# Kernel optimization log

Hardware: AMD Instinct MI355X
Metric: run time of the kernel (lower is better)

Reference implementation:

```python
import jax, jax.numpy as jnp
import numpy as np

B, S, D, H = 2, 48, 256, 8
DH = D // H  # depth per head = 32
N = S * S    # flattened pair sequence length = 2304


def setup_inputs() -> dict:
    key = jax.random.key(0)
    ks = jax.random.split(key, 9)
    std = 1.0 / np.sqrt(D)
    x = jax.random.normal(ks[0], (B, S, S, D), dtype=jnp.float32)
    Wq = jax.random.normal(ks[1], (D, D), dtype=jnp.float32) * std
    Wk = jax.random.normal(ks[2], (D, D), dtype=jnp.float32) * std
    Wv = jax.random.normal(ks[3], (D, D), dtype=jnp.float32) * std
    Wo = jax.random.normal(ks[4], (D, D), dtype=jnp.float32) * std
    bq = jnp.zeros((D,), jnp.float32)
    bk = jnp.zeros((D,), jnp.float32)
    bv = jnp.zeros((D,), jnp.float32)
    bo = jnp.zeros((D,), jnp.float32)
    return {"pair_representation": x, "Wq": Wq, "bq": bq, "Wk": Wk, "bk": bk,
            "Wv": Wv, "bv": bv, "Wo": Wo, "bo": bo}


def reference(pair_representation, Wq, bq, Wk, bk, Wv, bv, Wo, bo):
    x = pair_representation.reshape(B, N, D)  # flatten (S,S) -> N

    def heads(t):  # (B,N,D) -> (B,H,N,DH)
        return t.reshape(B, N, H, DH).transpose(0, 2, 1, 3)

    q = heads(x @ Wq + bq)
    k = heads(x @ Wk + bk)
    v = heads(x @ Wv + bv)

    scale = 1.0 / jnp.sqrt(jnp.asarray(DH, jnp.float32))
    logits = jnp.einsum('bhnd,bhmd->bhnm', q, k) * scale  # (B,H,N,N)
    attn = jax.nn.softmax(logits, axis=-1)
    ctx = jnp.einsum('bhnm,bhmd->bhnd', attn, v)
    ctx = ctx.transpose(0, 2, 1, 3).reshape(B, N, D)
    return ctx @ Wo + bo  # (B, N, D)
```

## Files before the change

kernel.cpp:

```cpp
#include <hip/hip_runtime.h>
#include <math.h>

#define B 2
#define S 48
#define D 256
#define H 8
#define DH 32
#define N (S*S)
#define BN (B*N)
#define BH (B*H)
#define KS 6
#define KPZ (N/KS)
#define NE ((size_t)BN*D)
#define BHN (BH*N)

typedef _Float16 half8 __attribute__((ext_vector_type(8)));
typedef _Float16 half4_t __attribute__((ext_vector_type(4)));
typedef unsigned short ushort8_t __attribute__((ext_vector_type(8)));
typedef float floatx4 __attribute__((ext_vector_type(4)));

__device__ __forceinline__ void split8(const float* v, half8* hi, half8* lo) {
    #pragma unroll
    for (int j = 0; j < 8; j++) {
        _Float16 h = (_Float16)v[j];
        (*hi)[j] = h;
        (*lo)[j] = (_Float16)(v[j] - (float)h);
    }
}

__global__ __launch_bounds__(256) void proj_kernel(
    const float* __restrict__ x,
    const float* __restrict__ Wq, const float* __restrict__ bq,
    const float* __restrict__ Wk, const float* __restrict__ bk,
    const float* __restrict__ Wv, const float* __restrict__ bv,
    _Float16* __restrict__ qbuf, _Float16* __restrict__ kbuf,
    _Float16* __restrict__ vtbuf)
{
    __shared__ __align__(16) _Float16 AhS[64 * 72];
    __shared__ __align__(16) _Float16 AlS[64 * 72];
    __shared__ __align__(16) _Float16 BhS[64 * 72];
    __shared__ __align__(16) _Float16 BlS[64 * 72];

    const int z = blockIdx.z;
    const float* W    = (z == 0) ? Wq : (z == 1) ? Wk : Wv;
    const float* bias = (z == 0) ? bq : (z == 1) ? bk : bv;
    const float scale = (z == 0) ? rsqrtf((float)DH) * 1.44269504f : 1.0f;

    const int t = threadIdx.x;
    const int wv2 = t >> 6, lane = t & 63, l15 = lane & 15, quad = lane >> 4;
    const int rowb = blockIdx.x * 64;
    const int colb = blockIdx.y * 64;
    floatx4 acc[4] = {{0,0,0,0},{0,0,0,0},{0,0,0,0},{0,0,0,0}};

    for (int kb0 = 0; kb0 < D; kb0 += 64) {
        __syncthreads();
        #pragma unroll
        for (int i = 0; i < 2; i++) {
            int idx = i * 2048 + t * 8;
            int r = idx >> 6, c = idx & 63;
            const float* xp = x + (size_t)(rowb + r) * D + kb0 + c;
            float4 x0 = *(const float4*)xp;
            float4 x1 = *(const float4*)(xp + 4);
            float v[8] = {x0.x, x0.y, x0.z, x0.w, x1.x, x1.y, x1.z, x1.w};
            half8 hi, lo;
            split8(v, &hi, &lo);
            *(half8*)(AhS + r * 72 + c) = hi;
            *(half8*)(AlS + r * 72 + c) = lo;
        }
        #pragma unroll
        for (int i = 0; i < 2; i++) {
            int u = i * 256 + t;
            int cc = u & 63, k0 = (u >> 6) * 8;
            float v[8];
            #pragma unroll
            for (int j = 0; j < 8; j++)
                v[j] = W[(size_t)(kb0 + k0 + j) * D + colb + cc];
            half8 hi, lo;
            split8(v, &hi, &lo);
            *(half8*)(BhS + cc * 72 + k0) = hi;
            *(half8*)(BlS + cc * 72 + k0) = lo;
        }
        __syncthreads();
        #pragma unroll
        for (int ksx = 0; ksx < 2; ksx++) {
            half8 ah = *(const half8*)(AhS + (wv2 * 16 + l15) * 72 + ksx * 32 + quad * 8);
            half8 al = *(const half8*)(AlS + (wv2 * 16 + l15) * 72 + ksx * 32 + quad * 8);
            #pragma unroll
            for (int cg = 0; cg < 4; cg++) {
                half8 bh8 = *(const half8*)(BhS + (cg * 16 + l15) * 72 + ksx * 32 + quad * 8);
                half8 bl8 = *(const half8*)(BlS + (cg * 16 + l15) * 72 + ksx * 32 + quad * 8);
                acc[cg] = __builtin_amdgcn_mfma_f32_16x16x32_f16(ah, bh8, acc[cg], 0, 0, 0);
                acc[cg] = __builtin_amdgcn_mfma_f32_16x16x32_f16(al, bh8, acc[cg], 0, 0, 0);
                acc[cg] = __builtin_amdgcn_mfma_f32_16x16x32_f16(ah, bl8, acc[cg], 0, 0, 0);
            }
        }
    }

    const int bb = (rowb >= N) ? 1 : 0;
    #pragma unroll
    for (int cg = 0; cg < 4; cg++) {
        int col = colb + cg * 16 + l15;
        int hh = col >> 5, dh = col & 31;
        float bs = bias[col];
        if (z < 2) {
            _Float16* op = (z == 0) ? qbuf : kbuf;
            #pragma unroll
            for (int r = 0; r < 4; r++) {
                int n = rowb + wv2 * 16 + quad * 4 + r - bb * N;
                float v = (acc[cg][r] + bs) * scale;
                op[((size_t)(bb * H + hh) * N + n) * DH + dh] = (_Float16)v;
            }
        } else {
            int n0 = rowb + wv2 * 16 + quad * 4 - bb * N;
            half4_t pk;
            #pragma unroll
            for (int r = 0; r < 4; r++) pk[r] = (_Float16)(acc[cg][r] + bs);
            *(half4_t*)(vtbuf + ((size_t)(bb * H + hh) * DH + dh) * N + n0) = pk;
        }
    }
}

__global__ __launch_bounds__(256) void attn_kernel(
    const _Float16* __restrict__ qbuf, const _Float16* __restrict__ kbuf,
    const _Float16* __restrict__ vtbuf,
    float* __restrict__ ctx_part, float* __restrict__ lpart)
{
    __shared__ __align__(16) _Float16 Ks[64 * 40];
    __shared__ __align__(16) _Float16 Vt[32 * 72];

    const int t = threadIdx.x;
    const int wv2 = t >> 6, lane = t & 63, l15 = lane & 15, quad = lane >> 4;
    const int bh = blockIdx.y, kz = blockIdx.z;
    const int qbase = blockIdx.x * 128 + wv2 * 32;

    half8 bq8[2];
    #pragma unroll
    for (int qg = 0; qg < 2; qg++)
        bq8[qg] = *(const half8*)(qbuf +
            ((size_t)bh * N + qbase + qg * 16 + l15) * DH + quad * 8);

    floatx4 acc[2][2] = {{{0,0,0,0},{0,0,0,0}},{{0,0,0,0},{0,0,0,0}}};
    float lsum[2] = {0.f, 0.f};

    const int skey = t >> 2, sd0 = (t & 3) * 8;
    const int svd = t >> 3, svk = (t & 7) * 8;

    for (int it = 0; it < KPZ / 64; it++) {
        const int key0 = kz * KPZ + it * 64;
        __syncthreads();
        *(ushort8_t*)(Ks + skey * 40 + sd0) =
            *(const ushort8_t*)(kbuf + ((size_t)bh * N + key0 + skey) * DH + sd0);
        *(ushort8_t*)(Vt + svd * 72 + svk) =
            *(const ushort8_t*)(vtbuf + ((size_t)bh * DH + svd) * N + key0 + svk);
        __syncthreads();

        #pragma unroll
        for (int kg = 0; kg < 4; kg++) {
            half8 ka = *(const half8*)(Ks + (kg * 16 + l15) * 40 + quad * 8);
            half4_t va0 = *(const half4_t*)(Vt + l15 * 72 + kg * 16 + quad * 4);
            half4_t va1 = *(const half4_t*)(Vt + (16 + l15) * 72 + kg * 16 + quad * 4);
            #pragma unroll
            for (int qg = 0; qg < 2; qg++) {
                floatx4 s = {0, 0, 0, 0};
                s = __builtin_amdgcn_mfma_f32_16x16x32_f16(ka, bq8[qg], s, 0, 0, 0);
                half4_t pf;
                #pragma unroll
                for (int r = 0; r < 4; r++) {
                    float p = exp2f(s[r]);
                    lsum[qg] += p;
                    pf[r] = (_Float16)p;
                }
                acc[qg][0] = __builtin_amdgcn_mfma_f32_16x16x16f16(va0, pf, acc[qg][0], 0, 0, 0);
                acc[qg][1] = __builtin_amdgcn_mfma_f32_16x16x16f16(va1, pf, acc[qg][1], 0, 0, 0);
            }
        }
    }

    const int bb = bh >> 3, hh = bh & 7;
    #pragma unroll
    for (int qg = 0; qg < 2; qg++) {
        float ls = lsum[qg];
        ls += __shfl_xor(ls, 16);
        ls += __shfl_xor(ls, 32);
        int q = qbase + qg * 16 + l15;
        if (quad == 0) lpart[(size_t)kz * BHN + bh * N + q] = ls;
        float* crow = ctx_part + (size_t)kz * NE + ((size_t)bb * N + q) * D + hh * DH;
        *(floatx4*)(crow + quad * 4)      = acc[qg][0];
        *(floatx4*)(crow + 16 + quad * 4) = acc[qg][1];
    }
}

__global__ __launch_bounds__(256) void outproj_kernel(
    const float* __restrict__ ctx_part, const float* __restrict__ lpart,
    const float* __restrict__ Wo, const float* __restrict__ bo,
    float* __restrict__ out)
{
    __shared__ __align__(16) _Float16 AhS[64 * 72];
    __shared__ __align__(16) _Float16 AlS[64 * 72];
    __shared__ __align__(16) _Float16 BhS[64 * 72];
    __shared__ __align__(16) _Float16 BlS[64 * 72];

    const int t = threadIdx.x;
    const int wv2 = t >> 6, lane = t & 63, l15 = lane & 15, quad = lane >> 4;
    const int rowb = blockIdx.x * 64;
    const int colb = blockIdx.y * 64;
    floatx4 acc[4] = {{0,0,0,0},{0,0,0,0},{0,0,0,0},{0,0,0,0}};

    for (int kb0 = 0; kb0 < D; kb0 += 64) {
        __syncthreads();
        #pragma unroll
        for (int i = 0; i < 2; i++) {
            int idx = i * 2048 + t * 8;
            int r = idx >> 6, c = idx & 63;
            int row = rowb + r;
            int kcol = kb0 + c;
            int bb = (row >= N) ? 1 : 0;
            int n = row - bb * N;
            int bhn = (bb * H + (kcol >> 5)) * N + n;
            float ls = 0.f;
            #pragma unroll
            for (int zz = 0; zz < KS; zz++) ls += lpart[(size_t)zz * BHN + bhn];
            float inv = 1.0f / ls;
            float v[8] = {};
            #pragma unroll
            for (int zz = 0; zz < KS; zz++) {
                const float* pp = ctx_part + (size_t)zz * NE + (size_t)row * D + kcol;
                float4 p0 = *(const float4*)pp;
                float4 p1 = *(const float4*)(pp + 4);
                v[0] += p0.x; v[1] += p0.y; v[2] += p0.z; v[3] += p0.w;
                v[4] += p1.x; v[5] += p1.y; v[6] += p1.z; v[7] += p1.w;
            }
            #pragma unroll
            for (int j = 0; j < 8; j++) v[j] *= inv;
            half8 hi, lo;
            split8(v, &hi, &lo);
            *(half8*)(AhS + r * 72 + c) = hi;
            *(half8*)(AlS + r * 72 + c) = lo;
        }
        #pragma unroll
        for (int i = 0; i < 2; i++) {
            int u = i * 256 + t;
            int cc = u & 63, k0 = (u >> 6) * 8;
            float v[8];
            #pragma unroll
            for (int j = 0; j < 8; j++)
                v[j] = Wo[(size_t)(kb0 + k0 + j) * D + colb + cc];
            half8 hi, lo;
            split8(v, &hi, &lo);
            *(half8*)(BhS + cc * 72 + k0) = hi;
            *(half8*)(BlS + cc * 72 + k0) = lo;
        }
        __syncthreads();
        #pragma unroll
        for (int ksx = 0; ksx < 2; ksx++) {
            half8 ah = *(const half8*)(AhS + (wv2 * 16 + l15) * 72 + ksx * 32 + quad * 8);
            half8 al = *(const half8*)(AlS + (wv2 * 16 + l15) * 72 + ksx * 32 + quad * 8);
            #pragma unroll
            for (int cg = 0; cg < 4; cg++) {
                half8 bh8 = *(const half8*)(BhS + (cg * 16 + l15) * 72 + ksx * 32 + quad * 8);
                half8 bl8 = *(const half8*)(BlS + (cg * 16 + l15) * 72 + ksx * 32 + quad * 8);
                acc[cg] = __builtin_amdgcn_mfma_f32_16x16x32_f16(ah, bh8, acc[cg], 0, 0, 0);
                acc[cg] = __builtin_amdgcn_mfma_f32_16x16x32_f16(al, bh8, acc[cg], 0, 0, 0);
                acc[cg] = __builtin_amdgcn_mfma_f32_16x16x32_f16(ah, bl8, acc[cg], 0, 0, 0);
            }
        }
    }

    #pragma unroll
    for (int cg = 0; cg < 4; cg++) {
        int col = colb + cg * 16 + l15;
        float bs = bo[col];
        #pragma unroll
        for (int r = 0; r < 4; r++) {
            int row = rowb + wv2 * 16 + quad * 4 + r;
            out[(size_t)row * D + col] = acc[cg][r] + bs;
        }
    }
}

extern "C" void kernel_launch(void* const* d_in, const int* in_sizes, int n_in,
                              void* d_out, int out_size, void* d_ws, size_t ws_size,
                              hipStream_t stream)
{
    const float* x  = (const float*)d_in[0];
    const float* Wq = (const float*)d_in[1];
    const float* bq = (const float*)d_in[2];
    const float* Wk = (const float*)d_in[3];
    const float* bk = (const float*)d_in[4];
    const float* Wv = (const float*)d_in[5];
    const float* bv = (const float*)d_in[6];
    const float* Wo = (const float*)d_in[7];
    const float* bo = (const float*)d_in[8];
    float* out = (float*)d_out;

    float* ctx_part = (float*)d_ws;
    float* lpart    = ctx_part + (size_t)KS * NE;
    _Float16* qbuf  = (_Float16*)(lpart + (size_t)KS * BHN);
    _Float16* kbuf  = qbuf + NE;
    _Float16* vtbuf = kbuf + NE;

    proj_kernel<<<dim3(BN / 64, D / 64, 3), 256, 0, stream>>>(
        x, Wq, bq, Wk, bk, Wv, bv, qbuf, kbuf, vtbuf);

    attn_kernel<<<dim3(N / 128, BH, KS), 256, 0, stream>>>(
        qbuf, kbuf, vtbuf, ctx_part, lpart);

    outproj_kernel<<<dim3(BN / 64, D / 64), 256, 0, stream>>>(
        ctx_part, lpart, Wo, bo, out);
}
```

Baseline: 146.3 us.

## Store attention partials in fp16 and load A operands directly into registers

The attention kernel now writes its per-split context partials as fp16 rather than fp32, which halves the workspace traffic between the attention and output-projection kernels. Both GEMM kernels drop the shared-memory staging of the A operand and have each lane load its own row slice from global memory, splitting it into hi/lo fp16 in registers. The output projection precomputes the inverse softmax denominators per row and head into shared memory once, instead of recomputing them every k-block. The trade-off is lost precision in the unnormalized partial sums stored as fp16, plus less coalesced direct global loads for the A tiles.

```diff
diff --git a/kernel.cpp b/kernel.cpp
--- a/kernel.cpp
+++ b/kernel.cpp
@@ -36,8 +36,6 @@
     _Float16* __restrict__ qbuf, _Float16* __restrict__ kbuf,
     _Float16* __restrict__ vtbuf)
 {
-    __shared__ __align__(16) _Float16 AhS[64 * 72];
-    __shared__ __align__(16) _Float16 AlS[64 * 72];
     __shared__ __align__(16) _Float16 BhS[64 * 72];
     __shared__ __align__(16) _Float16 BlS[64 * 72];
 
@@ -50,23 +48,11 @@
     const int wv2 = t >> 6, lane = t & 63, l15 = lane & 15, quad = lane >> 4;
     const int rowb = blockIdx.x * 64;
     const int colb = blockIdx.y * 64;
+    const int grow = rowb + wv2 * 16 + l15;
     floatx4 acc[4] = {{0,0,0,0},{0,0,0,0},{0,0,0,0},{0,0,0,0}};
 
     for (int kb0 = 0; kb0 < D; kb0 += 64) {
         __syncthreads();
-        #pragma unroll
-        for (int i = 0; i < 2; i++) {
-            int idx = i * 2048 + t * 8;
-            int r = idx >> 6, c = idx & 63;
-            const float* xp = x + (size_t)(rowb + r) * D + kb0 + c;
-            float4 x0 = *(const float4*)xp;
-            float4 x1 = *(const float4*)(xp + 4);
-            float v[8] = {x0.x, x0.y, x0.z, x0.w, x1.x, x1.y, x1.z, x1.w};
-            half8 hi, lo;
-            split8(v, &hi, &lo);
-            *(half8*)(AhS + r * 72 + c) = hi;
-            *(half8*)(AlS + r * 72 + c) = lo;
-        }
         #pragma unroll
         for (int i = 0; i < 2; i++) {
             int u = i * 256 + t;
@@ -83,8 +69,12 @@
         __syncthreads();
         #pragma unroll
         for (int ksx = 0; ksx < 2; ksx++) {
-            half8 ah = *(const half8*)(AhS + (wv2 * 16 + l15) * 72 + ksx * 32 + quad * 8);
-            half8 al = *(const half8*)(AlS + (wv2 * 16 + l15) * 72 + ksx * 32 + quad * 8);
+            const float* xp = x + (size_t)grow * D + kb0 + ksx * 32 + quad * 8;
+            float4 x0 = *(const float4*)xp;
+            float4 x1 = *(const float4*)(xp + 4);
+            float v[8] = {x0.x, x0.y, x0.z, x0.w, x1.x, x1.y, x1.z, x1.w};
+            half8 ah, al;
+            split8(v, &ah, &al);
             #pragma unroll
             for (int cg = 0; cg < 4; cg++) {
                 half8 bh8 = *(const half8*)(BhS + (cg * 16 + l15) * 72 + ksx * 32 + quad * 8);
@@ -123,7 +113,7 @@
 __global__ __launch_bounds__(256) void attn_kernel(
     const _Float16* __restrict__ qbuf, const _Float16* __restrict__ kbuf,
     const _Float16* __restrict__ vtbuf,
-    float* __restrict__ ctx_part, float* __restrict__ lpart)
+    _Float16* __restrict__ ctx_part, float* __restrict__ lpart)
 {
     __shared__ __align__(16) _Float16 Ks[64 * 40];
     __shared__ __align__(16) _Float16 Vt[32 * 72];
@@ -184,59 +174,50 @@
         ls += __shfl_xor(ls, 32);
         int q = qbase + qg * 16 + l15;
         if (quad == 0) lpart[(size_t)kz * BHN + bh * N + q] = ls;
-        float* crow = ctx_part + (size_t)kz * NE + ((size_t)bb * N + q) * D + hh * DH;
-        *(floatx4*)(crow + quad * 4)      = acc[qg][0];
-        *(floatx4*)(crow + 16 + quad * 4) = acc[qg][1];
+        _Float16* crow = ctx_part + (size_t)kz * NE + ((size_t)bb * N + q) * D + hh * DH;
+        half4_t c0, c1;
+        #pragma unroll
+        for (int r = 0; r < 4; r++) {
+            c0[r] = (_Float16)acc[qg][0][r];
+            c1[r] = (_Float16)acc[qg][1][r];
+        }
+        *(half4_t*)(crow + quad * 4)      = c0;
+        *(half4_t*)(crow + 16 + quad * 4) = c1;
     }
 }
 
 __global__ __launch_bounds__(256) void outproj_kernel(
-    const float* __restrict__ ctx_part, const float* __restrict__ lpart,
+    const _Float16* __restrict__ ctx_part, const float* __restrict__ lpart,
     const float* __restrict__ Wo, const float* __restrict__ bo,
     float* __restrict__ out)
 {
-    __shared__ __align__(16) _Float16 AhS[64 * 72];
-    __shared__ __align__(16) _Float16 AlS[64 * 72];
     __shared__ __align__(16) _Float16 BhS[64 * 72];
     __shared__ __align__(16) _Float16 BlS[64 * 72];
+    __shared__ float Linv[64 * 8];
 
     const int t = threadIdx.x;
     const int wv2 = t >> 6, lane = t & 63, l15 = lane & 15, quad = lane >> 4;
     const int rowb = blockIdx.x * 64;
     const int colb = blockIdx.y * 64;
+    const int grow = rowb + wv2 * 16 + l15;
+
+    #pragma unroll
+    for (int i = 0; i < 2; i++) {
+        int idx = i * 256 + t;
+        int r = idx >> 3, hh = idx & 7;
+        int row = rowb + r;
+        int bb = (row >= N) ? 1 : 0;
+        int bhn = (bb * H + hh) * N + (row - bb * N);
+        float ls = 0.f;
+        #pragma unroll
+        for (int zz = 0; zz < KS; zz++) ls += lpart[(size_t)zz * BHN + bhn];
+        Linv[idx] = 1.0f / ls;
+    }
+
     floatx4 acc[4] = {{0,0,0,0},{0,0,0,0},{0,0,0,0},{0,0,0,0}};
 
     for (int kb0 = 0; kb0 < D; kb0 += 64) {
         __syncthreads();
-        #pragma unroll
-        for (int i = 0; i < 2; i++) {
-            int idx = i * 2048 + t * 8;
-            int r = idx >> 6, c = idx & 63;
-            int row = rowb + r;
-            int kcol = kb0 + c;
-            int bb = (row >= N) ? 1 : 0;
-            int n = row - bb * N;
-            int bhn = (bb * H + (kcol >> 5)) * N + n;
-            float ls = 0.f;
-            #pragma unroll
-            for (int zz = 0; zz < KS; zz++) ls += lpart[(size_t)zz * BHN + bhn];
-            float inv = 1.0f / ls;
-            float v[8] = {};
-            #pragma unroll
-            for (int zz = 0; zz < KS; zz++) {
-                const float* pp = ctx_part + (size_t)zz * NE + (size_t)row * D + kcol;
-                float4 p0 = *(const float4*)pp;
-                float4 p1 = *(const float4*)(pp + 4);
-                v[0] += p0.x; v[1] += p0.y; v[2] += p0.z; v[3] += p0.w;
-                v[4] += p1.x; v[5] += p1.y; v[6] += p1.z; v[7] += p1.w;
-            }
-            #pragma unroll
-            for (int j = 0; j < 8; j++) v[j] *= inv;
-            half8 hi, lo;
-            split8(v, &hi, &lo);
-            *(half8*)(AhS + r * 72 + c) = hi;
-            *(half8*)(AlS + r * 72 + c) = lo;
-        }
         #pragma unroll
         for (int i = 0; i < 2; i++) {
             int u = i * 256 + t;
@@ -253,8 +234,19 @@
         __syncthreads();
         #pragma unroll
         for (int ksx = 0; ksx < 2; ksx++) {
-            half8 ah = *(const half8*)(AhS + (wv2 * 16 + l15) * 72 + ksx * 32 + quad * 8);
-            half8 al = *(const half8*)(AlS + (wv2 * 16 + l15) * 72 + ksx * 32 + quad * 8);
+            const int kcol = kb0 + ksx * 32 + quad * 8;
+            float linv = Linv[(wv2 * 16 + l15) * 8 + (kcol >> 5)];
+            float v[8] = {};
+            #pragma unroll
+            for (int zz = 0; zz < KS; zz++) {
+                half8 h = *(const half8*)(ctx_part + (size_t)zz * NE + (size_t)grow * D + kcol);
+                #pragma unroll
+                for (int j = 0; j < 8; j++) v[j] += (float)h[j];
+            }
+            #pragma unroll
+            for (int j = 0; j < 8; j++) v[j] *= linv;
+            half8 ah, al;
+            split8(v, &ah, &al);
             #pragma unroll
             for (int cg = 0; cg < 4; cg++) {
                 half8 bh8 = *(const half8*)(BhS + (cg * 16 + l15) * 72 + ksx * 32 + quad * 8);
@@ -293,8 +285,8 @@
     const float* bo = (const float*)d_in[8];
     float* out = (float*)d_out;
 
-    float* ctx_part = (float*)d_ws;
-    float* lpart    = ctx_part + (size_t)KS * NE;
+    _Float16* ctx_part = (_Float16*)d_ws;
+    float* lpart    = (float*)(ctx_part + (size_t)KS * NE);
     _Float16* qbuf  = (_Float16*)(lpart + (size_t)KS * BHN);
     _Float16* kbuf  = qbuf + NE;
     _Float16* vtbuf = kbuf + NE;
```

After: 133.9 us. 8.5% less time.
